# Performance work log

Hardware: AMD Instinct MI355X
Metric: run time of the kernel (lower is better)

Reference implementation:

```python
import jax, jax.numpy as jnp
import numpy as np

N_QUBITS = 12
DIM = 2 ** N_QUBITS  # 4096
N_LAYERS = 3
N_LABELS = 28
B = 1024
IN_DIM = 768

# PennyLane default.qubit convention: wire 0 is the most-significant bit.
_idx = np.arange(DIM)
_bits = (_idx[:, None] >> (N_QUBITS - 1 - np.arange(N_QUBITS))) & 1
_Z = (1.0 - 2.0 * _bits).astype(np.float32)  # (DIM, 12): eigenvalues of Z_q per basis state
_ZZ = np.stack([_Z[:, i] * _Z[:, i + 1] for i in range(N_QUBITS - 1)], axis=1)  # (DIM, 11)


def _apply_1q(state, U, q):
    # state: (B, DIM) complex; U: (2,2) shared or (B,2,2) per-sample
    b = state.shape[0]
    left, right = 2 ** q, 2 ** (N_QUBITS - q - 1)
    s = state.reshape(b, left, 2, right)
    if U.ndim == 2:
        s = jnp.einsum('ab,kxbj->kxaj', U, s)
    else:
        s = jnp.einsum('kab,kxbj->kxaj', U, s)
    return s.reshape(b, DIM)


def _apply_cnot(state, c, t):
    b = state.shape[0]
    s = state.reshape((b,) + (2,) * N_QUBITS)
    s = jnp.moveaxis(s, (c + 1, t + 1), (-2, -1))
    # flip target amplitudes where control bit == 1
    s = jnp.stack([s[..., 0, :], s[..., 1, ::-1]], axis=-2)
    s = jnp.moveaxis(s, (-2, -1), (c + 1, t + 1))
    return s.reshape(b, DIM)


def _ry_mats(angles):
    # angles: (B, 12) -> (B, 12, 2, 2) complex RY matrices
    c, s = jnp.cos(angles / 2), jnp.sin(angles / 2)
    U = jnp.stack([jnp.stack([c, -s], -1), jnp.stack([s, c], -1)], -2)
    return U.astype(jnp.complex64)


def _rot_mats(w):
    # w: (12, 3) -> (12, 2, 2); qml.Rot(phi, theta, omega) = RZ(omega) RY(theta) RZ(phi)
    phi, theta, omega = w[:, 0], w[:, 1], w[:, 2]
    c = jnp.cos(theta / 2).astype(jnp.complex64)
    s = jnp.sin(theta / 2).astype(jnp.complex64)
    a = jnp.exp(-0.5j * (phi + omega)) * c
    bb = -jnp.exp(0.5j * (phi - omega)) * s
    cc = jnp.exp(-0.5j * (phi - omega)) * s
    d = jnp.exp(0.5j * (phi + omega)) * c
    return jnp.stack([jnp.stack([a, bb], -1), jnp.stack([cc, d], -1)], -2)


def _forward(x, W1, b1, ln_g, ln_b, W2, b2, qws, scales, biases):
    # --- DimensionalityReduction MLP (eval mode: dropout = identity) ---
    h = x @ W1.T + b1                                   # (B, 24)
    mu = h.mean(-1, keepdims=True)
    var = ((h - mu) ** 2).mean(-1, keepdims=True)
    h = (h - mu) / jnp.sqrt(var + 1e-5) * ln_g + ln_b   # LayerNorm
    h = jax.nn.relu(h)
    angles = jnp.tanh(h @ W2.T + b2)                    # (B, 12) in [-1, 1]

    # --- batched 12-qubit state-vector simulation ---
    state = jnp.zeros((angles.shape[0], DIM), jnp.complex64).at[:, 0].set(1.0)
    Ury = _ry_mats(angles)                              # (B, 12, 2, 2)
    for l in range(N_LAYERS):
        for q in range(N_QUBITS):                       # AngleEmbedding (RY, per sample)
            state = _apply_1q(state, Ury[:, q], q)
        R = _rot_mats(qws[l][0])                        # StronglyEntanglingLayers: Rot per qubit
        for q in range(N_QUBITS):
            state = _apply_1q(state, R[q], q)
        for q in range(N_QUBITS):                       # CNOT ring, range 1
            state = _apply_cnot(state, q, (q + 1) % N_QUBITS)

    probs = state.real ** 2 + state.imag ** 2           # (B, DIM)
    eZ = probs @ jnp.asarray(_Z)                        # (B, 12)
    eZZ = probs @ jnp.asarray(_ZZ)                      # (B, 11)
    eX = []
    for q in range(N_LABELS - N_QUBITS - (N_QUBITS - 1)):  # 5 PauliX observables
        left, right = 2 ** q, 2 ** (N_QUBITS - q - 1)
        s = state.reshape(-1, left, 2, right)
        eX.append(2 * jnp.sum(s[:, :, 0, :].real * s[:, :, 1, :].real
                              + s[:, :, 0, :].imag * s[:, :, 1, :].imag, axis=(1, 2)))
    exps = jnp.concatenate([eZ, eZZ, jnp.stack(eX, -1)], axis=1)  # (B, 28)
    return exps * scales + biases


def setup_inputs() -> dict:
    key = jax.random.key(0)
    ks = jax.random.split(key, 8)
    x = jax.random.normal(ks[0], (B, IN_DIM), jnp.float32)
    W1 = jax.random.normal(ks[1], (2 * N_QUBITS, IN_DIM), jnp.float32) * 0.05
    b1 = jnp.zeros((2 * N_QUBITS,), jnp.float32)
    ln_g = jnp.ones((2 * N_QUBITS,), jnp.float32)
    ln_b = jnp.zeros((2 * N_QUBITS,), jnp.float32)
    W2 = jax.random.normal(ks[2], (N_QUBITS, 2 * N_QUBITS), jnp.float32) * 0.2
    b2 = jnp.zeros((N_QUBITS,), jnp.float32)
    qw0 = jax.random.normal(ks[3], (1, N_QUBITS, 3), jnp.float32) * 0.1
    qw1 = jax.random.normal(ks[4], (1, N_QUBITS, 3), jnp.float32) * 0.1
    qw2 = jax.random.normal(ks[5], (1, N_QUBITS, 3), jnp.float32) * 0.1
    scales = jnp.ones((N_LABELS,), jnp.float32)
    biases = jnp.zeros((N_LABELS,), jnp.float32)
    return {"x": x, "W1": W1, "b1": b1, "ln_g": ln_g, "ln_b": ln_b, "W2": W2,
            "b2": b2, "qw0": qw0, "qw1": qw1, "qw2": qw2,
            "scales": scales, "biases": biases}


def reference(x, W1, b1, ln_g, ln_b, W2, b2, qw0, qw1, qw2, scales, biases):
    return _forward(x, W1, b1, ln_g, ln_b, W2, b2, (qw0, qw1, qw2), scales, biases)
```

## Files before the change

kernel.cpp:

```cpp
#include <hip/hip_runtime.h>
#include <math.h>

#define NQ   12
#define BLK  64
#define IND  768
#define HD   24
#define NOBS 28
#define CSTR 20

typedef float    f32x2 __attribute__((ext_vector_type(2)));
typedef float    f32x4 __attribute__((ext_vector_type(4)));
typedef __fp16   f16x2 __attribute__((ext_vector_type(2)));
typedef _Float16 h8    __attribute__((ext_vector_type(8)));

__device__ __forceinline__ unsigned pkrtz(float x, float y) {
    f16x2 h = __builtin_amdgcn_cvt_pkrtz(x, y);
    unsigned u; __builtin_memcpy(&u, &h, 4); return u;
}
__device__ __forceinline__ f32x2 unpack2(unsigned u) {
    f16x2 h; __builtin_memcpy(&h, &u, 4);
    f32x2 v; v.x = (float)h.x; v.y = (float)h.y; return v;
}
__device__ __forceinline__ f32x2 pk_cmul(f32x2 m, f32x2 u) {
    f32x2 r;
    asm("v_pk_mul_f32 %0, %1, %2 op_sel:[0,0] op_sel_hi:[0,1]"
        : "=v"(r) : "v"(m), "v"(u));
    asm("v_pk_fma_f32 %0, %1, %2, %0 op_sel:[1,1,0] op_sel_hi:[1,0,1] neg_lo:[0,1,0]"
        : "+v"(r) : "v"(m), "v"(u));
    return r;
}
__device__ __forceinline__ void pk_fma_plain(f32x2& acc, f32x2 a, f32x2 b) {
    asm("v_pk_fma_f32 %0, %1, %2, %0" : "+v"(acc) : "v"(a), "v"(b));
}
__device__ __forceinline__ h8 as_h8(uint4 u) { h8 r; __builtin_memcpy(&r, &u, 16); return r; }

__device__ __forceinline__ int pfx12(int y) { y ^= y >> 1; y ^= y >> 2; y ^= y >> 4; y ^= y >> 8; return y; }
__device__ __forceinline__ int pfx8 (int y) { y ^= y >> 1; y ^= y >> 2; y ^= y >> 4; return y; }

template<int LI, int G, int WM>
__device__ __forceinline__ void gstage(unsigned* st, const float GM[3][NQ][8], int l) {
    const int a  = l & 15;
    const int mb = (l >> 4) * 4;

    unsigned A0u[4], A1u[4];
    #pragma unroll
    for (int bi = 0; bi < 4; ++bi) {
        const int bq = mb + bi;
        f32x2 u;
        {
            const float* F = GM[LI][11 - 4*G];
            const int off = (a & 1) * 4 + (bq & 1) * 2;
            u.x = F[off]; u.y = F[off + 1];
        }
        #pragma unroll
        for (int p = 1; p < 4; ++p) {
            const float* F = GM[LI][11 - 4*G - p];
            const int off = ((a >> p) & 1) * 4 + ((bq >> p) & 1) * 2;
            f32x2 e; e.x = F[off]; e.y = F[off + 1];
            u = pk_cmul(e, u);
        }
        A0u[bi] = pkrtz(u.x, -u.y);
        A1u[bi] = pkrtz(u.y,  u.x);
    }

    __syncthreads();
    uint4 Bf[16];
    #pragma unroll
    for (int t = 0; t < 16; ++t)
        Bf[t] = *(const uint4*)(st + (16 * t + a) * CSTR + mb);
    asm volatile("" ::: "memory");

    uint4 A04; A04.x = A0u[0]; A04.y = A0u[1]; A04.z = A0u[2]; A04.w = A0u[3];
    uint4 A14; A14.x = A1u[0]; A14.y = A1u[1]; A14.z = A1u[2]; A14.w = A1u[3];
    const h8 A0 = as_h8(A04), A1 = as_h8(A14);

    int TL = 0;
    if (WM >= 2) TL = pfx12(mb << 8);
    const int CTJ[4] = {0, 0x1FF, 0x3FF, 0x200};

    #pragma unroll
    for (int t = 0; t < 16; ++t) {
        f32x4 c0 = {0.f, 0.f, 0.f, 0.f}, c1 = {0.f, 0.f, 0.f, 0.f};
        const h8 Bh = as_h8(Bf[t]);
        c0 = __builtin_amdgcn_mfma_f32_16x16x32_f16(A0, Bh, c0, 0, 0, 0);
        c1 = __builtin_amdgcn_mfma_f32_16x16x32_f16(A1, Bh, c1, 0, 0, 0);
        const int n  = 16 * t + a;
        const int TN = (WM >= 2) ? (pfx8(n) ^ TL) : 0;
        #pragma unroll
        for (int j = 0; j < 4; ++j) {
            const int m = mb + j;
            int addr;
            if (WM == 0)      addr = (m | (n & 0xF0)) * CSTR + (n & 15);
            else if (WM == 1) addr = ((n & 15) | (m << 4)) * CSTR + (n >> 4);
            else {
                const int tt = TN ^ CTJ[j];
                const int jp = tt ^ ((tt & 1) << 11);
                addr = (WM == 2) ? ((jp >> 4) * CSTR + (jp & 15))
                                 : ((jp & 255) * CSTR + (jp >> 8));
            }
            st[addr] = pkrtz(c0[j], c1[j]);
        }
    }
}

__global__ void __launch_bounds__(BLK) pqm_kernel(
    const float* __restrict__ x,   const float* __restrict__ W1,
    const float* __restrict__ b1,  const float* __restrict__ ln_g,
    const float* __restrict__ ln_b,const float* __restrict__ W2,
    const float* __restrict__ b2,  const float* __restrict__ qw0,
    const float* __restrict__ qw1, const float* __restrict__ qw2,
    const float* __restrict__ scales, const float* __restrict__ biases,
    float* __restrict__ out)
{
    __shared__ unsigned st[256 * CSTR];
    __shared__ float GM[3][NQ][8];
    __shared__ float hb[HD];
    __shared__ float ang[2 * NQ];
    __shared__ float obsl[NOBS];

    const int l   = threadIdx.x;
    const int row = blockIdx.x;

    float* xs = (float*)st;
    {
        const float4* xg = (const float4*)(x + row * IND);
        #pragma unroll
        for (int k = 0; k < 3; ++k)
            ((float4*)xs)[l + 64 * k] = xg[l + 64 * k];
    }
    __syncthreads();

    {
        int l8 = l & 7;
        #pragma unroll
        for (int rd = 0; rd < 3; ++rd) {
            int g = rd * 8 + (l >> 3);
            const float* wp = W1 + g * IND + l8 * 96;
            const float* xp = xs + l8 * 96;
            float acc = 0.f;
            #pragma unroll
            for (int j = 0; j < 24; ++j) {
                float4 w4 = *(const float4*)(wp + 4 * j);
                float4 a4 = *(const float4*)(xp + 4 * j);
                acc += a4.x * w4.x + a4.y * w4.y + a4.z * w4.z + a4.w * w4.w;
            }
            acc += __shfl_down(acc, 4, 8);
            acc += __shfl_down(acc, 2, 8);
            acc += __shfl_down(acc, 1, 8);
            if (l8 == 0) hb[g] = acc + b1[g];
        }
    }
    __syncthreads();

    if (l < NQ) {
        float mu = 0.f;
        #pragma unroll
        for (int j = 0; j < HD; ++j) mu += hb[j];
        mu *= (1.f / HD);
        float var = 0.f;
        #pragma unroll
        for (int j = 0; j < HD; ++j) { float d = hb[j] - mu; var += d * d; }
        var *= (1.f / HD);
        float rinv = 1.f / sqrtf(var + 1e-5f);
        float acc = b2[l];
        #pragma unroll
        for (int j = 0; j < HD; ++j) {
            float hn = (hb[j] - mu) * rinv * ln_g[j] + ln_b[j];
            acc += fmaxf(hn, 0.f) * W2[l * HD + j];
        }
        float a = tanhf(acc);
        ang[l]      = cosf(0.5f * a);
        ang[NQ + l] = sinf(0.5f * a);
    } else if (l < 48) {
        int li = (l - 12) / NQ, q = (l - 12) % NQ;
        const float* qw = (li == 0) ? qw0 : ((li == 1) ? qw1 : qw2);
        float phi = qw[q*3+0], th = qw[q*3+1], om = qw[q*3+2];
        float c = cosf(0.5f*th), s = sinf(0.5f*th);
        float sp, cp, sm, cm;
        sincosf(0.5f*(phi+om), &sp, &cp);
        sincosf(0.5f*(phi-om), &sm, &cm);
        float* R = GM[li][q];
        R[0] =  cp*c;  R[1] = -sp*c;
        R[2] = -cm*s;  R[3] = -sm*s;
        R[4] =  cm*s;  R[5] = -sm*s;
        R[6] =  cp*c;  R[7] =  sp*c;
    }
    __syncthreads();
    if (l < 36) {
        int li = l / NQ, q = l % NQ;
        float* R = GM[li][q];
        float r0=R[0],r1=R[1],r2=R[2],r3=R[3],r4=R[4],r5=R[5],r6=R[6],r7=R[7];
        float cr = ang[q], sr = ang[NQ + q];
        R[0] =  r0*cr + r2*sr;  R[1] =  r1*cr + r3*sr;
        R[2] = -r0*sr + r2*cr;  R[3] = -r1*sr + r3*cr;
        R[4] =  r4*cr + r6*sr;  R[5] =  r5*cr + r7*sr;
        R[6] = -r4*sr + r6*cr;  R[7] = -r5*sr + r7*cr;
    }
    __syncthreads();

    {
        f32x2 v[64];
        f32x2 lf; lf.x = 1.f; lf.y = 0.f;
        #pragma unroll
        for (int u = 0; u < 6; ++u) {
            const float* F = GM[0][5 - u];
            const int bit = (l >> u) & 1;
            f32x2 e; e.x = F[bit * 4]; e.y = F[bit * 4 + 1];
            lf = pk_cmul(e, lf);
        }
        {
            const float* F = GM[0][11];
            f32x2 e0; e0.x = F[0]; e0.y = F[1];
            f32x2 e1; e1.x = F[4]; e1.y = F[5];
            v[0] = pk_cmul(e0, lf); v[1] = pk_cmul(e1, lf);
        }
        #pragma unroll
        for (int b = 1; b < 6; ++b) {
            const float* F = GM[0][11 - b];
            f32x2 e0; e0.x = F[0]; e0.y = F[1];
            f32x2 e1; e1.x = F[4]; e1.y = F[5];
            #pragma unroll
            for (int r = 0; r < (1 << b); ++r) {
                v[r | (1 << b)] = pk_cmul(e1, v[r]);
                v[r]            = pk_cmul(e0, v[r]);
            }
        }
        const int TL6 = pfx12(l << 6);
        #pragma unroll
        for (int r = 0; r < 64; ++r) {
            int tr = r ^ (r >> 1); tr ^= tr >> 2; tr ^= tr >> 4;
            const int tt = TL6 ^ tr;
            const int jp = tt ^ ((tt & 1) << 11);
            st[(jp >> 4) * CSTR + (jp & 15)] = pkrtz(v[r].x, v[r].y);
        }
    }

    gstage<1, 0, 0>(st, GM, l);
    gstage<1, 1, 1>(st, GM, l);
    gstage<1, 2, 2>(st, GM, l);
    gstage<2, 0, 0>(st, GM, l);
    gstage<2, 1, 1>(st, GM, l);
    gstage<2, 2, 3>(st, GM, l);
    __syncthreads();

    {
        f32x2 v[64];
        #pragma unroll
        for (int r = 0; r < 64; ++r) {
            const int n = ((r & 3) << 6) | l;
            v[r] = unpack2(st[n * CSTR + (r >> 2)]);
        }
        float ex[5];
        #pragma unroll
        for (int q = 0; q < 5; ++q) {
            f32x2 acc; acc.x = 0.f; acc.y = 0.f;
            #pragma unroll
            for (int r = 0; r < 64; ++r) pk_fma_plain(acc, v[r], v[r ^ (0x20 >> q)]);
            ex[q] = acc.x + acc.y;
        }
        #pragma unroll
        for (int r = 0; r < 64; ++r) v[r].x = v[r].x * v[r].x + v[r].y * v[r].y;
        #pragma unroll
        for (int lev = 0; lev < 6; ++lev) {
            const int m = 1 << lev;
            #pragma unroll
            for (int r = 0; r < 64; ++r)
                if (!(r & m)) {
                    float A = v[r].x, B = v[r | m].x;
                    v[r].x = A + B; v[r | m].x = A - B;
                }
        }
        auto wsum = [&](float s) {
            #pragma unroll
            for (int d = 1; d < 64; d <<= 1) s += __shfl_xor(s, d, 64);
            return s;
        };
        float ch = v[0].x;
        #pragma unroll
        for (int lev = 0; lev < 6; ++lev) {
            float o = __shfl_xor(ch, 1 << lev, 64);
            ch = (l & (1 << lev)) ? (o - ch) : (ch + o);
        }
        float z0 = wsum(v[0x20].x), z1 = wsum(v[0x10].x), z2 = wsum(v[8].x);
        float z3 = wsum(v[4].x),    z4 = wsum(v[2].x),    z5 = wsum(v[1].x);
        float zz0 = wsum(v[0x30].x), zz1 = wsum(v[0x18].x), zz2 = wsum(v[0xC].x);
        float zz3 = wsum(v[6].x),    zz4 = wsum(v[3].x);
        float zz5 = wsum((l & 0x20) ? -v[1].x : v[1].x);
        float e0 = wsum(ex[0]), e1 = wsum(ex[1]), e2 = wsum(ex[2]);
        float e3 = wsum(ex[3]), e4 = wsum(ex[4]);

        if (l == 0) {
            obsl[0] = z0; obsl[1] = z1; obsl[2] = z2;
            obsl[3] = z3; obsl[4] = z4; obsl[5] = z5;
            obsl[12] = zz0; obsl[13] = zz1; obsl[14] = zz2;
            obsl[15] = zz3; obsl[16] = zz4; obsl[17] = zz5;
            obsl[23] = e0; obsl[24] = e1; obsl[25] = e2;
            obsl[26] = e3; obsl[27] = e4;
        }
        if (l == 32) obsl[6]  = ch;
        if (l == 16) obsl[7]  = ch;
        if (l == 8)  obsl[8]  = ch;
        if (l == 4)  obsl[9]  = ch;
        if (l == 2)  obsl[10] = ch;
        if (l == 1)  obsl[11] = ch;
        if (l == 48) obsl[18] = ch;
        if (l == 24) obsl[19] = ch;
        if (l == 12) obsl[20] = ch;
        if (l == 6)  obsl[21] = ch;
        if (l == 3)  obsl[22] = ch;
    }
    __syncthreads();

    if (l < NOBS)
        out[row * NOBS + l] = obsl[l] * scales[l] + biases[l];
}

extern "C" void kernel_launch(void* const* d_in, const int* in_sizes, int n_in,
                              void* d_out, int out_size, void* d_ws, size_t ws_size,
                              hipStream_t stream) {
    const int Bn = in_sizes[0] / IND;
    pqm_kernel<<<dim3(Bn), dim3(BLK), 0, stream>>>(
        (const float*)d_in[0], (const float*)d_in[1], (const float*)d_in[2],
        (const float*)d_in[3], (const float*)d_in[4], (const float*)d_in[5],
        (const float*)d_in[6], (const float*)d_in[7], (const float*)d_in[8],
        (const float*)d_in[9], (const float*)d_in[10], (const float*)d_in[11],
        (float*)d_out);
}
```

Measured before the change: 33.27 us.

## Split each sample's state-vector simulation across four wavefronts per block

Block size grows from one wavefront to four. The MFMA gate stages, the initial product-state build and the observable reductions are each divided across the wavefronts, so every wave handles a quarter of the tiles and amplitudes. Per-wave partial observables go to shared memory and are combined with sign masks at the end, and the MLP and rotation-matrix setup now run in parallel across more threads. The cost is an extra block barrier per gate stage plus cross-wave reduction, in exchange for fewer registers per thread and more parallelism per sample.

```diff
diff --git a/kernel.cpp b/kernel.cpp
--- a/kernel.cpp
+++ b/kernel.cpp
@@ -2,7 +2,7 @@
 #include <math.h>
 
 #define NQ   12
-#define BLK  64
+#define BLK  256
 #define IND  768
 #define HD   24
 #define NOBS 28
@@ -38,7 +38,8 @@
 __device__ __forceinline__ int pfx8 (int y) { y ^= y >> 1; y ^= y >> 2; y ^= y >> 4; return y; }
 
 template<int LI, int G, int WM>
-__device__ __forceinline__ void gstage(unsigned* st, const float GM[3][NQ][8], int l) {
+__device__ __forceinline__ void gstage(unsigned* st, const float GM[3][NQ][8],
+                                       int l, int w) {
     const int a  = l & 15;
     const int mb = (l >> 4) * 4;
 
@@ -64,11 +65,11 @@
     }
 
     __syncthreads();
-    uint4 Bf[16];
+    uint4 Bf[4];
     #pragma unroll
-    for (int t = 0; t < 16; ++t)
-        Bf[t] = *(const uint4*)(st + (16 * t + a) * CSTR + mb);
-    asm volatile("" ::: "memory");
+    for (int tt = 0; tt < 4; ++tt)
+        Bf[tt] = *(const uint4*)(st + (16 * (4*w + tt) + a) * CSTR + mb);
+    __syncthreads();
 
     uint4 A04; A04.x = A0u[0]; A04.y = A0u[1]; A04.z = A0u[2]; A04.w = A0u[3];
     uint4 A14; A14.x = A1u[0]; A14.y = A1u[1]; A14.z = A1u[2]; A14.w = A1u[3];
@@ -79,12 +80,12 @@
     const int CTJ[4] = {0, 0x1FF, 0x3FF, 0x200};
 
     #pragma unroll
-    for (int t = 0; t < 16; ++t) {
+    for (int tt = 0; tt < 4; ++tt) {
         f32x4 c0 = {0.f, 0.f, 0.f, 0.f}, c1 = {0.f, 0.f, 0.f, 0.f};
-        const h8 Bh = as_h8(Bf[t]);
+        const h8 Bh = as_h8(Bf[tt]);
         c0 = __builtin_amdgcn_mfma_f32_16x16x32_f16(A0, Bh, c0, 0, 0, 0);
         c1 = __builtin_amdgcn_mfma_f32_16x16x32_f16(A1, Bh, c1, 0, 0, 0);
-        const int n  = 16 * t + a;
+        const int n  = 16 * (4*w + tt) + a;
         const int TN = (WM >= 2) ? (pfx8(n) ^ TL) : 0;
         #pragma unroll
         for (int j = 0; j < 4; ++j) {
@@ -93,8 +94,8 @@
             if (WM == 0)      addr = (m | (n & 0xF0)) * CSTR + (n & 15);
             else if (WM == 1) addr = ((n & 15) | (m << 4)) * CSTR + (n >> 4);
             else {
-                const int tt = TN ^ CTJ[j];
-                const int jp = tt ^ ((tt & 1) << 11);
+                const int tz = TN ^ CTJ[j];
+                const int jp = tz ^ ((tz & 1) << 11);
                 addr = (WM == 2) ? ((jp >> 4) * CSTR + (jp & 15))
                                  : ((jp & 255) * CSTR + (jp >> 8));
             }
@@ -116,25 +117,20 @@
     __shared__ float GM[3][NQ][8];
     __shared__ float hb[HD];
     __shared__ float ang[2 * NQ];
-    __shared__ float obsl[NOBS];
-
-    const int l   = threadIdx.x;
+    __shared__ float wpar[4][24];
+
+    const int t   = threadIdx.x;
+    const int w   = t >> 6;
+    const int l   = t & 63;
     const int row = blockIdx.x;
 
     float* xs = (float*)st;
+    if (t < 192) ((float4*)xs)[t] = ((const float4*)(x + row * IND))[t];
+    __syncthreads();
+
     {
-        const float4* xg = (const float4*)(x + row * IND);
-        #pragma unroll
-        for (int k = 0; k < 3; ++k)
-            ((float4*)xs)[l + 64 * k] = xg[l + 64 * k];
-    }
-    __syncthreads();
-
-    {
-        int l8 = l & 7;
-        #pragma unroll
-        for (int rd = 0; rd < 3; ++rd) {
-            int g = rd * 8 + (l >> 3);
+        int g = t >> 3, l8 = t & 7;
+        if (g < HD) {
             const float* wp = W1 + g * IND + l8 * 96;
             const float* xp = xs + l8 * 96;
             float acc = 0.f;
@@ -148,11 +144,24 @@
             acc += __shfl_down(acc, 2, 8);
             acc += __shfl_down(acc, 1, 8);
             if (l8 == 0) hb[g] = acc + b1[g];
-        }
-    }
-    __syncthreads();
-
-    if (l < NQ) {
+        } else if (t >= 192 && t < 228) {
+            int u = t - 192; int li = u / NQ, q = u % NQ;
+            const float* qw = (li == 0) ? qw0 : ((li == 1) ? qw1 : qw2);
+            float phi = qw[q*3+0], th = qw[q*3+1], om = qw[q*3+2];
+            float c = cosf(0.5f*th), s = sinf(0.5f*th);
+            float sp, cp, sm, cm;
+            sincosf(0.5f*(phi+om), &sp, &cp);
+            sincosf(0.5f*(phi-om), &sm, &cm);
+            float* R = GM[li][q];
+            R[0] =  cp*c;  R[1] = -sp*c;
+            R[2] = -cm*s;  R[3] = -sm*s;
+            R[4] =  cm*s;  R[5] = -sm*s;
+            R[6] =  cp*c;  R[7] =  sp*c;
+        }
+    }
+    __syncthreads();
+
+    if (t < NQ) {
         float mu = 0.f;
         #pragma unroll
         for (int j = 0; j < HD; ++j) mu += hb[j];
@@ -162,32 +171,19 @@
         for (int j = 0; j < HD; ++j) { float d = hb[j] - mu; var += d * d; }
         var *= (1.f / HD);
         float rinv = 1.f / sqrtf(var + 1e-5f);
-        float acc = b2[l];
+        float acc = b2[t];
         #pragma unroll
         for (int j = 0; j < HD; ++j) {
             float hn = (hb[j] - mu) * rinv * ln_g[j] + ln_b[j];
-            acc += fmaxf(hn, 0.f) * W2[l * HD + j];
+            acc += fmaxf(hn, 0.f) * W2[t * HD + j];
         }
         float a = tanhf(acc);
-        ang[l]      = cosf(0.5f * a);
-        ang[NQ + l] = sinf(0.5f * a);
-    } else if (l < 48) {
-        int li = (l - 12) / NQ, q = (l - 12) % NQ;
-        const float* qw = (li == 0) ? qw0 : ((li == 1) ? qw1 : qw2);
-        float phi = qw[q*3+0], th = qw[q*3+1], om = qw[q*3+2];
-        float c = cosf(0.5f*th), s = sinf(0.5f*th);
-        float sp, cp, sm, cm;
-        sincosf(0.5f*(phi+om), &sp, &cp);
-        sincosf(0.5f*(phi-om), &sm, &cm);
-        float* R = GM[li][q];
-        R[0] =  cp*c;  R[1] = -sp*c;
-        R[2] = -cm*s;  R[3] = -sm*s;
-        R[4] =  cm*s;  R[5] = -sm*s;
-        R[6] =  cp*c;  R[7] =  sp*c;
-    }
-    __syncthreads();
-    if (l < 36) {
-        int li = l / NQ, q = l % NQ;
+        ang[t]      = cosf(0.5f * a);
+        ang[NQ + t] = sinf(0.5f * a);
+    }
+    __syncthreads();
+    if (t < 36) {
+        int li = t / NQ, q = t % NQ;
         float* R = GM[li][q];
         float r0=R[0],r1=R[1],r2=R[2],r3=R[3],r4=R[4],r5=R[5],r6=R[6],r7=R[7];
         float cr = ang[q], sr = ang[NQ + q];
@@ -199,12 +195,12 @@
     __syncthreads();
 
     {
-        f32x2 v[64];
+        f32x2 v0[16];
         f32x2 lf; lf.x = 1.f; lf.y = 0.f;
         #pragma unroll
-        for (int u = 0; u < 6; ++u) {
-            const float* F = GM[0][5 - u];
-            const int bit = (l >> u) & 1;
+        for (int u = 0; u < 8; ++u) {
+            const float* F = GM[0][7 - u];
+            const int bit = (t >> u) & 1;
             f32x2 e; e.x = F[bit * 4]; e.y = F[bit * 4 + 1];
             lf = pk_cmul(e, lf);
         }
@@ -212,107 +208,131 @@
             const float* F = GM[0][11];
             f32x2 e0; e0.x = F[0]; e0.y = F[1];
             f32x2 e1; e1.x = F[4]; e1.y = F[5];
-            v[0] = pk_cmul(e0, lf); v[1] = pk_cmul(e1, lf);
-        }
-        #pragma unroll
-        for (int b = 1; b < 6; ++b) {
+            v0[0] = pk_cmul(e0, lf); v0[1] = pk_cmul(e1, lf);
+        }
+        #pragma unroll
+        for (int b = 1; b < 4; ++b) {
             const float* F = GM[0][11 - b];
             f32x2 e0; e0.x = F[0]; e0.y = F[1];
             f32x2 e1; e1.x = F[4]; e1.y = F[5];
             #pragma unroll
             for (int r = 0; r < (1 << b); ++r) {
-                v[r | (1 << b)] = pk_cmul(e1, v[r]);
-                v[r]            = pk_cmul(e0, v[r]);
+                v0[r | (1 << b)] = pk_cmul(e1, v0[r]);
+                v0[r]            = pk_cmul(e0, v0[r]);
             }
         }
-        const int TL6 = pfx12(l << 6);
-        #pragma unroll
-        for (int r = 0; r < 64; ++r) {
-            int tr = r ^ (r >> 1); tr ^= tr >> 2; tr ^= tr >> 4;
-            const int tt = TL6 ^ tr;
-            const int jp = tt ^ ((tt & 1) << 11);
-            st[(jp >> 4) * CSTR + (jp & 15)] = pkrtz(v[r].x, v[r].y);
-        }
-    }
-
-    gstage<1, 0, 0>(st, GM, l);
-    gstage<1, 1, 1>(st, GM, l);
-    gstage<1, 2, 2>(st, GM, l);
-    gstage<2, 0, 0>(st, GM, l);
-    gstage<2, 1, 1>(st, GM, l);
-    gstage<2, 2, 3>(st, GM, l);
+        const int TL = pfx12(t << 4);
+        #pragma unroll
+        for (int r = 0; r < 16; ++r) {
+            const int tr = r ^ (r >> 1) ^ (r >> 2) ^ (r >> 3);
+            const int tz = TL ^ tr;
+            const int jp = tz ^ ((tz & 1) << 11);
+            st[(jp >> 4) * CSTR + (jp & 15)] = pkrtz(v0[r].x, v0[r].y);
+        }
+    }
+
+    gstage<1, 0, 0>(st, GM, l, w);
+    gstage<1, 1, 1>(st, GM, l, w);
+    gstage<1, 2, 2>(st, GM, l, w);
+    gstage<2, 0, 0>(st, GM, l, w);
+    gstage<2, 1, 1>(st, GM, l, w);
+    gstage<2, 2, 3>(st, GM, l, w);
     __syncthreads();
 
     {
-        f32x2 v[64];
-        #pragma unroll
-        for (int r = 0; r < 64; ++r) {
-            const int n = ((r & 3) << 6) | l;
-            v[r] = unpack2(st[n * CSTR + (r >> 2)]);
+        f32x2 v[16];
+        #pragma unroll
+        for (int i = 0; i < 4; ++i) {
+            uint4 raw = *(const uint4*)(st + t * CSTR + 4 * i);
+            v[4*i+0] = unpack2(raw.x); v[4*i+1] = unpack2(raw.y);
+            v[4*i+2] = unpack2(raw.z); v[4*i+3] = unpack2(raw.w);
         }
         float ex[5];
         #pragma unroll
-        for (int q = 0; q < 5; ++q) {
+        for (int q = 0; q < 4; ++q) {
             f32x2 acc; acc.x = 0.f; acc.y = 0.f;
-            #pragma unroll
-            for (int r = 0; r < 64; ++r) pk_fma_plain(acc, v[r], v[r ^ (0x20 >> q)]);
+            const int m = 8 >> q;
+            #pragma unroll
+            for (int r = 0; r < 16; ++r) pk_fma_plain(acc, v[r], v[r ^ m]);
             ex[q] = acc.x + acc.y;
         }
-        #pragma unroll
-        for (int r = 0; r < 64; ++r) v[r].x = v[r].x * v[r].x + v[r].y * v[r].y;
+        {
+            f32x2 acc; acc.x = 0.f; acc.y = 0.f;
+            #pragma unroll
+            for (int i = 0; i < 4; ++i) {
+                uint4 raw = *(const uint4*)(st + (t ^ 0x80) * CSTR + 4 * i);
+                f32x2 p0 = unpack2(raw.x), p1 = unpack2(raw.y);
+                f32x2 p2 = unpack2(raw.z), p3 = unpack2(raw.w);
+                pk_fma_plain(acc, v[4*i+0], p0); pk_fma_plain(acc, v[4*i+1], p1);
+                pk_fma_plain(acc, v[4*i+2], p2); pk_fma_plain(acc, v[4*i+3], p3);
+            }
+            ex[4] = acc.x + acc.y;
+        }
+
+        float pr[16];
+        #pragma unroll
+        for (int r = 0; r < 16; ++r) pr[r] = v[r].x * v[r].x + v[r].y * v[r].y;
+        #pragma unroll
+        for (int lev = 0; lev < 4; ++lev) {
+            const int m = 1 << lev;
+            #pragma unroll
+            for (int r = 0; r < 16; ++r)
+                if (!(r & m)) { float A = pr[r], B = pr[r | m]; pr[r] = A + B; pr[r | m] = A - B; }
+        }
+
+        float ch = pr[0];
         #pragma unroll
         for (int lev = 0; lev < 6; ++lev) {
-            const int m = 1 << lev;
-            #pragma unroll
-            for (int r = 0; r < 64; ++r)
-                if (!(r & m)) {
-                    float A = v[r].x, B = v[r | m].x;
-                    v[r].x = A + B; v[r | m].x = A - B;
-                }
+            float o = __shfl_xor(ch, 1 << lev, 64);
+            ch = (l & (1 << lev)) ? (o - ch) : (ch + o);
         }
         auto wsum = [&](float s) {
             #pragma unroll
             for (int d = 1; d < 64; d <<= 1) s += __shfl_xor(s, d, 64);
             return s;
         };
-        float ch = v[0].x;
-        #pragma unroll
-        for (int lev = 0; lev < 6; ++lev) {
-            float o = __shfl_xor(ch, 1 << lev, 64);
-            ch = (l & (1 << lev)) ? (o - ch) : (ch + o);
-        }
-        float z0 = wsum(v[0x20].x), z1 = wsum(v[0x10].x), z2 = wsum(v[8].x);
-        float z3 = wsum(v[4].x),    z4 = wsum(v[2].x),    z5 = wsum(v[1].x);
-        float zz0 = wsum(v[0x30].x), zz1 = wsum(v[0x18].x), zz2 = wsum(v[0xC].x);
-        float zz3 = wsum(v[6].x),    zz4 = wsum(v[3].x);
-        float zz5 = wsum((l & 0x20) ? -v[1].x : v[1].x);
+        float W8 = wsum(pr[8]),  W4 = wsum(pr[4]), W2 = wsum(pr[2]), W1 = wsum(pr[1]);
+        float WC = wsum(pr[12]), W6 = wsum(pr[6]), W3 = wsum(pr[3]);
         float e0 = wsum(ex[0]), e1 = wsum(ex[1]), e2 = wsum(ex[2]);
         float e3 = wsum(ex[3]), e4 = wsum(ex[4]);
 
-        if (l == 0) {
-            obsl[0] = z0; obsl[1] = z1; obsl[2] = z2;
-            obsl[3] = z3; obsl[4] = z4; obsl[5] = z5;
-            obsl[12] = zz0; obsl[13] = zz1; obsl[14] = zz2;
-            obsl[15] = zz3; obsl[16] = zz4; obsl[17] = zz5;
-            obsl[23] = e0; obsl[24] = e1; obsl[25] = e2;
-            obsl[26] = e3; obsl[27] = e4;
-        }
-        if (l == 32) obsl[6]  = ch;
-        if (l == 16) obsl[7]  = ch;
-        if (l == 8)  obsl[8]  = ch;
-        if (l == 4)  obsl[9]  = ch;
-        if (l == 2)  obsl[10] = ch;
-        if (l == 1)  obsl[11] = ch;
-        if (l == 48) obsl[18] = ch;
-        if (l == 24) obsl[19] = ch;
-        if (l == 12) obsl[20] = ch;
-        if (l == 6)  obsl[21] = ch;
-        if (l == 3)  obsl[22] = ch;
-    }
-    __syncthreads();
-
-    if (l < NOBS)
-        out[row * NOBS + l] = obsl[l] * scales[l] + biases[l];
+        if      (l == 0) {
+            wpar[w][0]  = ch;
+            wpar[w][12] = W8; wpar[w][13] = W4; wpar[w][14] = W2; wpar[w][15] = W1;
+            wpar[w][16] = WC; wpar[w][17] = W6; wpar[w][18] = W3;
+            wpar[w][19] = e0; wpar[w][20] = e1; wpar[w][21] = e2;
+            wpar[w][22] = e3; wpar[w][23] = e4;
+        }
+        else if (l == 32) wpar[w][1]  = ch;
+        else if (l == 16) wpar[w][2]  = ch;
+        else if (l == 8)  wpar[w][3]  = ch;
+        else if (l == 4)  wpar[w][4]  = ch;
+        else if (l == 2)  wpar[w][5]  = ch;
+        else if (l == 1)  wpar[w][6]  = ch;
+        else if (l == 48) wpar[w][7]  = ch;
+        else if (l == 24) wpar[w][8]  = ch;
+        else if (l == 12) wpar[w][9]  = ch;
+        else if (l == 6)  wpar[w][10] = ch;
+        else if (l == 3)  wpar[w][11] = ch;
+    }
+    __syncthreads();
+
+    if (t < NOBS) {
+        const int oslot[NOBS] = {12,13,14,15, 0,0,1,2,3,4,5,6,
+                                 16,17,18,15,0,1,7,8,9,10,11,
+                                 19,20,21,22,23};
+        const int omw[NOBS]   = {0,0,0,0, 2,1,0,0,0,0,0,0,
+                                 0,0,0,2,3,1,0,0,0,0,0,
+                                 0,0,0,0,0};
+        const int sl = oslot[t], mw = omw[t];
+        float s = 0.f;
+        #pragma unroll
+        for (int g = 0; g < 4; ++g) {
+            float p = wpar[g][sl];
+            s += (__popc(g & mw) & 1) ? -p : p;
+        }
+        out[row * NOBS + t] = s * scales[t] + biases[t];
+    }
 }
 
 extern "C" void kernel_launch(void* const* d_in, const int* in_sizes, int n_in,
```

Measured after the change: 29.06 us. -12.6%, faster.
